# Performance work log

Measured on AMD Instinct MI355X. Metric: run time of the kernel, lower is better.

## Reference

```python
import jax, jax.numpy as jnp
import numpy as np

N = 100000       # num nodes
E = 1600000      # num edges (before self loops)
IN = 128         # in_channels
H = 4            # heads (layer 1)
C = 64           # hidden_channels
BN_EPS = 1e-5
NEG_SLOPE = 0.2  # PyG GATConv default


def setup_inputs() -> dict:
    key = jax.random.key(0)
    ks = jax.random.split(key, 12)
    s = lambda k, shape: jax.random.normal(k, shape, jnp.float32) * 0.05
    return {
        "x": jax.random.normal(ks[0], (N, IN), jnp.float32),
        "edge_index": jax.random.randint(ks[1], (2, E), 0, N),
        # GATConv layer 1: in=128 -> 64 per head, 4 heads, concat
        "W1": s(ks[2], (IN, H * C)),
        "a_src1": s(ks[3], (H, C)),
        "a_dst1": s(ks[4], (H, C)),
        "b1": jnp.zeros((H * C,), jnp.float32),
        # BatchNorm1d(256), eval mode with default running stats
        "bn_gamma": jnp.ones((H * C,), jnp.float32),
        "bn_beta": jnp.zeros((H * C,), jnp.float32),
        # GATConv layer 2: 256 -> 1, heads=1, concat=False
        "W2": s(ks[5], (H * C, 1)),
        "a_src2": s(ks[6], (1, 1)),
        "a_dst2": s(ks[7], (1, 1)),
        "b2": jnp.zeros((1,), jnp.float32),
        # risk predictor MLP: Linear(1,64) -> ReLU -> Linear(64,1) -> Sigmoid
        "mlp_w1": s(ks[8], (1, C)),
        "mlp_b1": jnp.zeros((C,), jnp.float32),
        "mlp_w2": s(ks[9], (C, 1)),
        "mlp_b2": jnp.zeros((1,), jnp.float32),
    }


def gat_conv(x, W, a_s, a_d, b, src, dst, n, concat):
    """PyG-style GATConv (self loops already appended to src/dst)."""
    h_, c_ = a_s.shape
    h = (x @ W).reshape(n, h_, c_)                       # [N,H,C]
    alpha_src = jnp.einsum('nhc,hc->nh', h, a_s)          # [N,H]
    alpha_dst = jnp.einsum('nhc,hc->nh', h, a_d)          # [N,H]
    alpha = jax.nn.leaky_relu(alpha_src[src] + alpha_dst[dst], NEG_SLOPE)  # [E,H]
    # segment softmax over destination nodes (self loops guarantee nonempty segments)
    amax = jax.ops.segment_max(alpha, dst, num_segments=n)
    ex = jnp.exp(alpha - amax[dst])
    den = jax.ops.segment_sum(ex, dst, num_segments=n)
    coef = ex / den[dst]                                  # [E,H]
    out = jax.ops.segment_sum(h[src] * coef[..., None], dst, num_segments=n)  # [N,H,C]
    out = out.reshape(n, h_ * c_) if concat else out.mean(axis=1)
    return out + b


def reference(x, edge_index, W1, a_src1, a_dst1, b1, bn_gamma, bn_beta,
              W2, a_src2, a_dst2, b2, mlp_w1, mlp_b1, mlp_w2, mlp_b2):
    n = x.shape[0]
    loops = jnp.arange(n)
    src = jnp.concatenate([edge_index[0], loops])
    dst = jnp.concatenate([edge_index[1], loops])

    h = gat_conv(x, W1, a_src1, a_dst1, b1, src, dst, n, concat=True)   # [N,256]
    # BatchNorm1d eval: running_mean=0, running_var=1
    h = h / jnp.sqrt(jnp.float32(1.0 + BN_EPS)) * bn_gamma + bn_beta
    h = jax.nn.elu(h)
    # dropout is identity in eval mode
    h = gat_conv(h, W2, a_src2, a_dst2, b2, src, dst, n, concat=False)  # [N,1]

    risk = jax.nn.relu(h @ mlp_w1 + mlp_b1)
    risk = jax.nn.sigmoid(risk @ mlp_w2 + mlp_b2)                        # [N,1]
    return risk
```

## Files before the change

### kernel.cpp

```cpp
#include <hip/hip_runtime.h>
#include <math.h>

#define NSL 0.2f
#define BSH 8
#define CAP 4608
#define ECHUNK 4096
#define MAXNB 512

typedef __attribute__((ext_vector_type(8))) short bf16x8;
typedef __attribute__((ext_vector_type(4))) float f32x4;
typedef __attribute__((ext_vector_type(2))) float floatx2;

__device__ __forceinline__ unsigned short f2b(float f){
  unsigned int u = __builtin_bit_cast(unsigned int, f);
  u = (u + 0x7FFFu + ((u >> 16) & 1u)) >> 16;
  return (unsigned short)u;
}

__global__ void k_binit(int* gCur, int NB){
  int i = blockIdx.x*blockDim.x + threadIdx.x;
  if (i < NB) gCur[i] = i*CAP;
}

__global__ __launch_bounds__(256) void k_bucket(const int* __restrict__ esrc, const int* __restrict__ edst,
                                                int E, int NB, int* gCur, uint2* __restrict__ ebuf){
  __shared__ int hist[MAXNB];
  __shared__ int base[MAXNB];
  int t = threadIdx.x;
  for (int i=t;i<NB;i+=256) hist[i] = 0;
  __syncthreads();
  int e0 = blockIdx.x*ECHUNK;
  int srcv[16], dstv[16];
  #pragma unroll
  for (int j=0;j<16;j++){
    int e = e0 + t + j*256;
    if (e < E){ srcv[j] = esrc[e]; dstv[j] = edst[e]; atomicAdd(&hist[dstv[j]>>BSH], 1); }
    else dstv[j] = -1;
  }
  __syncthreads();
  for (int i=t;i<NB;i+=256){
    int h = hist[i];
    base[i] = h > 0 ? atomicAdd(&gCur[i], h) : 0;
    hist[i] = 0;
  }
  __syncthreads();
  #pragma unroll
  for (int j=0;j<16;j++){
    if (dstv[j] >= 0){
      int b = dstv[j]>>BSH;
      int pos = base[b] + atomicAdd(&hist[b], 1);
      if (pos < (b+1)*CAP)
        ebuf[pos] = (uint2){ (unsigned)srcv[j], (unsigned)dstv[j] };
    }
  }
}

__global__ __launch_bounds__(256) void k_csr(const int* __restrict__ gCur, const uint2* __restrict__ ebuf,
                                             int* __restrict__ rows, int* __restrict__ deg,
                                             int* __restrict__ csr, int N){
  __shared__ int lcnt[256];
  __shared__ int rofs[256];
  __shared__ int csr_l[CAP+256];
  int b = blockIdx.x, t = threadIdx.x;
  int node0 = b<<BSH;
  int nNodes = min(256, N - node0);
  int cnt_b = min(gCur[b] - b*CAP, CAP);
  lcnt[t] = 0;
  __syncthreads();
  const uint2* eb = ebuf + (size_t)b*CAP;
  for (int i=t;i<cnt_b;i+=256) atomicAdd(&lcnt[eb[i].y & 255], 1);
  __syncthreads();
  int v = (t < nNodes) ? (lcnt[t] + 1) : 0;
  rofs[t] = v; __syncthreads();
  #pragma unroll
  for (int o=1;o<256;o<<=1){
    int x = (t>=o) ? rofs[t-o] : 0; __syncthreads();
    rofs[t] += x; __syncthreads();
  }
  int excl = rofs[t] - v;
  if (t < nNodes) csr_l[excl] = node0 + t;
  lcnt[t] = excl + 1;
  __syncthreads();
  for (int i=t;i<cnt_b;i+=256){
    uint2 e = eb[i];
    int pos = atomicAdd(&lcnt[e.y & 255], 1);
    csr_l[pos] = (int)e.x;
  }
  __syncthreads();
  int total = rofs[255];
  int gbase = b*(CAP+256);
  for (int i=t;i<total;i+=256) csr[gbase+i] = csr_l[i];
  if (t < nNodes){ rows[node0+t] = gbase + excl; deg[node0+t] = v; }
}

__global__ void k_prep_x(const float* __restrict__ x, unsigned short* __restrict__ xb, int total8){
  int i = blockIdx.x*blockDim.x + threadIdx.x;
  if (i >= total8) return;
  size_t off = (size_t)i*8;
  float4 a = *(const float4*)&x[off];
  float4 b = *(const float4*)&x[off+4];
  ushort4 lo = { f2b(a.x), f2b(a.y), f2b(a.z), f2b(a.w) };
  ushort4 hi = { f2b(b.x), f2b(b.y), f2b(b.z), f2b(b.w) };
  *(ushort4*)&xb[off]   = lo;
  *(ushort4*)&xb[off+4] = hi;
}

__global__ __launch_bounds__(256) void k_prep_w(const float* __restrict__ W, unsigned short* __restrict__ wt){
  int ch = threadIdx.x;
  for (int k=0;k<128;k++) wt[ch*128 + k] = f2b(W[k*256 + ch]);
}

__global__ __launch_bounds__(256) void k_gemm1(const unsigned short* __restrict__ w1t,
                                               const unsigned short* __restrict__ xb,
                                               const float* __restrict__ a_s1,
                                               const float* __restrict__ a_d1,
                                               unsigned char* __restrict__ h1f8,
                                               float* __restrict__ asrc, float* __restrict__ adst,
                                               int N){
  int tid = threadIdx.x;
  int lane = tid & 63, w = tid >> 6;
  int g = lane >> 4, nr = lane & 15;
  int n0 = blockIdx.x*64;

  f32x4 acc[4][4] = {};
  int node_f[4]; bool val_f[4];
  #pragma unroll
  for (int fn=0;fn<4;fn++){ node_f[fn] = n0 + fn*16 + nr; val_f[fn] = node_f[fn] < N; }

  #pragma unroll
  for (int s=0;s<4;s++){
    int ks = s*32;
    bf16x8 af[4], bf[4];
    #pragma unroll
    for (int fm=0;fm<4;fm++){
      int ch = w*64 + fm*16 + nr;
      const ushort4 lo = *(const ushort4*)(w1t + ch*128 + ks + 4*g);
      const ushort4 hi = *(const ushort4*)(w1t + ch*128 + ks + 16 + 4*g);
      af[fm] = (bf16x8){ (short)lo.x,(short)lo.y,(short)lo.z,(short)lo.w,
                         (short)hi.x,(short)hi.y,(short)hi.z,(short)hi.w };
    }
    #pragma unroll
    for (int fn=0;fn<4;fn++){
      ushort4 lo = {0,0,0,0}, hi = {0,0,0,0};
      if (val_f[fn]){
        const unsigned short* xp = xb + (size_t)node_f[fn]*128 + ks + 4*g;
        lo = *(const ushort4*)xp;
        hi = *(const ushort4*)(xp + 16);
      }
      bf[fn] = (bf16x8){ (short)lo.x,(short)lo.y,(short)lo.z,(short)lo.w,
                         (short)hi.x,(short)hi.y,(short)hi.z,(short)hi.w };
    }
    #pragma unroll
    for (int fm=0;fm<4;fm++)
      #pragma unroll
      for (int fn=0;fn<4;fn++)
        acc[fm][fn] = __builtin_amdgcn_mfma_f32_16x16x32_bf16(af[fm], bf[fn], acc[fm][fn], 0, 0, 0);
  }

  float ps[4] = {0.f,0.f,0.f,0.f}, pd[4] = {0.f,0.f,0.f,0.f};
  #pragma unroll
  for (int fm=0;fm<4;fm++){
    int cb = w*64 + fm*16 + g*4;
    float4 av = *(const float4*)&a_s1[cb];
    float4 dv = *(const float4*)&a_d1[cb];
    #pragma unroll
    for (int fn=0;fn<4;fn++){
      f32x4 c = acc[fm][fn];
      if (val_f[fn]){
        int u = __builtin_amdgcn_cvt_pk_fp8_f32(c[0], c[1], 0, false);
        u = __builtin_amdgcn_cvt_pk_fp8_f32(c[2], c[3], u, true);
        *(unsigned int*)(h1f8 + (size_t)node_f[fn]*256 + cb) = (unsigned int)u;
      }
      ps[fn] += c[0]*av.x + c[1]*av.y + c[2]*av.z + c[3]*av.w;
      pd[fn] += c[0]*dv.x + c[1]*dv.y + c[2]*dv.z + c[3]*dv.w;
    }
  }
  #pragma unroll
  for (int fn=0;fn<4;fn++){
    ps[fn] += __shfl_xor(ps[fn], 16); ps[fn] += __shfl_xor(ps[fn], 32);
    pd[fn] += __shfl_xor(pd[fn], 16); pd[fn] += __shfl_xor(pd[fn], 32);
    if (g == 0 && val_f[fn]){
      asrc[node_f[fn]*4 + w] = ps[fn];
      adst[node_f[fn]*4 + w] = pd[fn];
    }
  }
}

__global__ __launch_bounds__(256) void k_agg1(const int* __restrict__ rows, const int* __restrict__ deg,
                                              const int* __restrict__ csr,
                                              const unsigned char* __restrict__ h1f8,
                                              const float* __restrict__ asrc, const float* __restrict__ adst,
                                              const float* __restrict__ b1,
                                              const float* __restrict__ gamma, const float* __restrict__ beta,
                                              const float* __restrict__ W2,
                                              float* __restrict__ h2, int N){
  int lane = threadIdx.x & 63, wv = threadIdx.x >> 6;
  int node = blockIdx.x*4 + wv;
  if (node >= N) return;
  int slot = lane >> 4, l4 = lane & 15;
  int head = l4 >> 2;
  int rs = rows[node], d = deg[node];
  float adh = adst[node*4 + head];
  const uint4* h1u4 = (const uint4*)h1f8;
  float acc[16];
  #pragma unroll
  for (int j=0;j<16;j++) acc[j] = 0.f;
  float den = 0.f;
  int i = slot;
  if (i < d){
    int s = csr[rs+i];
    float aa = asrc[s*4 + head];
    uint4 v = h1u4[(size_t)s*16 + l4];
    while (true){
      int in = i + 4;
      bool hn = in < d;
      int sn = hn ? csr[rs+in] : 0;
      float al = aa + adh;
      al = (al > 0.f) ? al : NSL*al;
      float wgt = __expf(al);
      den += wgt;
      floatx2 f0 = __builtin_amdgcn_cvt_pk_f32_fp8(v.x, false);
      floatx2 f1 = __builtin_amdgcn_cvt_pk_f32_fp8(v.x, true);
      floatx2 f2 = __builtin_amdgcn_cvt_pk_f32_fp8(v.y, false);
      floatx2 f3 = __builtin_amdgcn_cvt_pk_f32_fp8(v.y, true);
      floatx2 f4 = __builtin_amdgcn_cvt_pk_f32_fp8(v.z, false);
      floatx2 f5 = __builtin_amdgcn_cvt_pk_f32_fp8(v.z, true);
      floatx2 f6 = __builtin_amdgcn_cvt_pk_f32_fp8(v.w, false);
      floatx2 f7 = __builtin_amdgcn_cvt_pk_f32_fp8(v.w, true);
      acc[0] += wgt*f0.x;  acc[1] += wgt*f0.y;  acc[2] += wgt*f1.x;  acc[3] += wgt*f1.y;
      acc[4] += wgt*f2.x;  acc[5] += wgt*f2.y;  acc[6] += wgt*f3.x;  acc[7] += wgt*f3.y;
      acc[8] += wgt*f4.x;  acc[9] += wgt*f4.y;  acc[10]+= wgt*f5.x;  acc[11]+= wgt*f5.y;
      acc[12]+= wgt*f6.x;  acc[13]+= wgt*f6.y;  acc[14]+= wgt*f7.x;  acc[15]+= wgt*f7.y;
      if (!hn) break;
      i = in;
      aa = asrc[sn*4 + head];
      v = h1u4[(size_t)sn*16 + l4];
    }
  }
  #pragma unroll
  for (int j=0;j<16;j++){ acc[j] += __shfl_xor(acc[j],16); acc[j] += __shfl_xor(acc[j],32); }
  den += __shfl_xor(den,16); den += __shfl_xor(den,32);
  float inv = 1.f/den;
  const float bsc = 0.99999500003749968f;
  int c = l4*16;
  float p = 0.f;
  #pragma unroll
  for (int q=0;q<4;q++){
    int cq = c + q*4;
    float4 bb = *(const float4*)&b1[cq];
    float4 gg = *(const float4*)&gamma[cq];
    float4 be = *(const float4*)&beta[cq];
    float4 w2 = *(const float4*)&W2[cq];
    float o0 = (acc[q*4+0]*inv + bb.x)*bsc*gg.x + be.x;
    float o1 = (acc[q*4+1]*inv + bb.y)*bsc*gg.y + be.y;
    float o2 = (acc[q*4+2]*inv + bb.z)*bsc*gg.z + be.z;
    float o3 = (acc[q*4+3]*inv + bb.w)*bsc*gg.w + be.w;
    o0 = (o0>0.f)?o0:(__expf(o0)-1.f); o1 = (o1>0.f)?o1:(__expf(o1)-1.f);
    o2 = (o2>0.f)?o2:(__expf(o2)-1.f); o3 = (o3>0.f)?o3:(__expf(o3)-1.f);
    p += o0*w2.x + o1*w2.y + o2*w2.z + o3*w2.w;
  }
  p += __shfl_xor(p,1); p += __shfl_xor(p,2); p += __shfl_xor(p,4); p += __shfl_xor(p,8);
  if (lane == 0) h2[node] = p;
}

__global__ __launch_bounds__(256) void k_agg2(const int* __restrict__ rows, const int* __restrict__ deg,
                       const int* __restrict__ csr, const float* __restrict__ h2,
                       const float* __restrict__ as2, const float* __restrict__ ad2,
                       const float* __restrict__ b2,
                       const float* __restrict__ mw1, const float* __restrict__ mb1,
                       const float* __restrict__ mw2, const float* __restrict__ mb2,
                       float* __restrict__ out, int N){
  int t = threadIdx.x;
  int g16 = t >> 4, l = t & 15;
  int n = blockIdx.x*16 + g16;
  if (n >= N) return;
  float a_s = as2[0], a_d = ad2[0];
  float hd = h2[n];
  float ad = hd * a_d;
  int rs = rows[n], d = deg[n];
  float den = 0.f, num = 0.f;
  for (int i=l;i<d;i+=16){
    int s = csr[rs+i];
    float hs = h2[s];
    float al = hs*a_s + ad;
    al = (al > 0.f) ? al : NSL*al;
    float w = __expf(al);
    den += w; num += w*hs;
  }
  #pragma unroll
  for (int o=1;o<16;o<<=1){ den += __shfl_xor(den,o); num += __shfl_xor(num,o); }
  float o2 = num/den + b2[0];
  float acc = 0.f;
  #pragma unroll
  for (int q=0;q<4;q++){
    int j = l + q*16;
    float r = fmaxf(o2*mw1[j] + mb1[j], 0.f);
    acc += r*mw2[j];
  }
  #pragma unroll
  for (int o=1;o<16;o<<=1) acc += __shfl_xor(acc,o);
  if (l == 0) out[n] = 1.f/(1.f + __expf(-(acc + mb2[0])));
}

extern "C" void kernel_launch(void* const* d_in, const int* in_sizes, int n_in,
                              void* d_out, int out_size, void* d_ws, size_t ws_size,
                              hipStream_t stream){
  const float* x   = (const float*)d_in[0];
  const int*   ei  = (const int*)  d_in[1];
  const float* W1  = (const float*)d_in[2];
  const float* as1 = (const float*)d_in[3];
  const float* ad1 = (const float*)d_in[4];
  const float* b1  = (const float*)d_in[5];
  const float* gam = (const float*)d_in[6];
  const float* bet = (const float*)d_in[7];
  const float* W2  = (const float*)d_in[8];
  const float* as2 = (const float*)d_in[9];
  const float* ad2 = (const float*)d_in[10];
  const float* b2  = (const float*)d_in[11];
  const float* mw1 = (const float*)d_in[12];
  const float* mb1 = (const float*)d_in[13];
  const float* mw2 = (const float*)d_in[14];
  const float* mb2 = (const float*)d_in[15];
  float* out = (float*)d_out;

  int N = in_sizes[0] / 128;
  int E = in_sizes[1] / 2;
  const int* esrc = ei;
  const int* edst = ei + E;
  int NB = (N + 255) >> 8;

  char* p = (char*)d_ws;
  auto alloc = [&](size_t bytes)->char*{ char* r = p; p += (bytes + 255) & ~(size_t)255; return r; };
  int*   deg   = (int*)  alloc((size_t)N*4);
  int*   rows  = (int*)  alloc((size_t)N*4);
  int*   gCur  = (int*)  alloc((size_t)NB*4);
  uint2* ebuf  = (uint2*)alloc((size_t)NB*CAP*8);
  int*   csr   = (int*)  alloc((size_t)NB*(CAP+256)*4);
  unsigned short* xb   = (unsigned short*)alloc((size_t)N*128*2);
  unsigned short* w1t  = (unsigned short*)alloc((size_t)256*128*2);
  unsigned char*  h1f8 = (unsigned char*) alloc((size_t)N*256);
  float* asrc  = (float*)alloc((size_t)N*4*4);
  float* adst  = (float*)alloc((size_t)N*4*4);
  float* h2    = (float*)alloc((size_t)N*4);

  k_binit<<<(NB+255)/256,256,0,stream>>>(gCur, NB);
  int nbA = (E + ECHUNK - 1)/ECHUNK;
  k_bucket<<<nbA,256,0,stream>>>(esrc, edst, E, NB, gCur, ebuf);
  k_csr   <<<NB,256,0,stream>>>(gCur, ebuf, rows, deg, csr, N);

  int total8 = (N*128)/8;
  k_prep_x<<<(total8+255)/256,256,0,stream>>>(x, xb, total8);
  k_prep_w<<<1,256,0,stream>>>(W1, w1t);

  k_gemm1<<<(N+63)/64,256,0,stream>>>(w1t, xb, as1, ad1, h1f8, asrc, adst, N);

  k_agg1 <<<(N+3)/4,256,0,stream>>>(rows, deg, csr, h1f8, asrc, adst, b1, gam, bet, W2, h2, N);

  k_agg2 <<<(N+15)/16,256,0,stream>>>(rows, deg, csr, h2, as2, ad2, b2, mw1, mb1, mw2, mb2, out, N);
}
```

Before: 256.8 us.

## Fuse x bf16 conversion into GEMM, retile per-wave nodes, packed FMA aggregation

Removes the separate x-to-bf16 pass by loading fp32 x directly in the GEMM and converting with packed bf16 instructions. The GEMM is retiled so each wave owns 16 nodes and all 256 channels, which lets it write all four attention logits per node as one float4. The W1 transpose kernel is parallelised across 128 blocks. The first aggregation loop uses packed FP32 FMA via inline asm, and leaky ReLU becomes a max. W1 fragments are now reloaded by every wave, and the 16 accumulators raise register pressure.

```diff
diff --git a/kernel.cpp b/kernel.cpp
--- a/kernel.cpp
+++ b/kernel.cpp
@@ -15,6 +15,12 @@
   unsigned int u = __builtin_bit_cast(unsigned int, f);
   u = (u + 0x7FFFu + ((u >> 16) & 1u)) >> 16;
   return (unsigned short)u;
+}
+__device__ __forceinline__ unsigned cvtpk_bf16(float a, float b){
+  unsigned r; asm("v_cvt_pk_bf16_f32 %0, %1, %2" : "=v"(r) : "v"(a), "v"(b)); return r;
+}
+__device__ __forceinline__ void pkfma(floatx2& a, floatx2 x, floatx2 w){
+  asm("v_pk_fma_f32 %0, %1, %2, %0" : "+v"(a) : "v"(x), "v"(w));
 }
 
 __global__ void k_binit(int* gCur, int NB){
@@ -93,96 +99,73 @@
   if (t < nNodes){ rows[node0+t] = gbase + excl; deg[node0+t] = v; }
 }
 
-__global__ void k_prep_x(const float* __restrict__ x, unsigned short* __restrict__ xb, int total8){
-  int i = blockIdx.x*blockDim.x + threadIdx.x;
-  if (i >= total8) return;
-  size_t off = (size_t)i*8;
-  float4 a = *(const float4*)&x[off];
-  float4 b = *(const float4*)&x[off+4];
-  ushort4 lo = { f2b(a.x), f2b(a.y), f2b(a.z), f2b(a.w) };
-  ushort4 hi = { f2b(b.x), f2b(b.y), f2b(b.z), f2b(b.w) };
-  *(ushort4*)&xb[off]   = lo;
-  *(ushort4*)&xb[off+4] = hi;
-}
-
 __global__ __launch_bounds__(256) void k_prep_w(const float* __restrict__ W, unsigned short* __restrict__ wt){
-  int ch = threadIdx.x;
-  for (int k=0;k<128;k++) wt[ch*128 + k] = f2b(W[k*256 + ch]);
+  int idx = blockIdx.x*256 + threadIdx.x;
+  int k = idx >> 8, ch = idx & 255;
+  wt[ch*128 + k] = f2b(W[idx]);
 }
 
 __global__ __launch_bounds__(256) void k_gemm1(const unsigned short* __restrict__ w1t,
-                                               const unsigned short* __restrict__ xb,
+                                               const float* __restrict__ x,
                                                const float* __restrict__ a_s1,
                                                const float* __restrict__ a_d1,
                                                unsigned char* __restrict__ h1f8,
-                                               float* __restrict__ asrc, float* __restrict__ adst,
+                                               float* __restrict__ as4, float* __restrict__ ad4,
                                                int N){
   int tid = threadIdx.x;
   int lane = tid & 63, w = tid >> 6;
   int g = lane >> 4, nr = lane & 15;
-  int n0 = blockIdx.x*64;
-
-  f32x4 acc[4][4] = {};
-  int node_f[4]; bool val_f[4];
-  #pragma unroll
-  for (int fn=0;fn<4;fn++){ node_f[fn] = n0 + fn*16 + nr; val_f[fn] = node_f[fn] < N; }
-
-  #pragma unroll
-  for (int s=0;s<4;s++){
-    int ks = s*32;
-    bf16x8 af[4], bf[4];
+  int node = blockIdx.x*64 + w*16 + nr;
+  bool val = node < N;
+
+  f32x4 acc[16] = {};
+  #pragma unroll
+  for (int ks=0;ks<4;ks++){
+    float4 xlo = make_float4(0,0,0,0), xhi = xlo;
+    if (val){
+      const float* xp = x + (size_t)node*128 + ks*32 + 4*g;
+      xlo = *(const float4*)xp;
+      xhi = *(const float4*)(xp + 16);
+    }
+    union { unsigned u[4]; bf16x8 v; } bb;
+    bb.u[0] = cvtpk_bf16(xlo.x, xlo.y);
+    bb.u[1] = cvtpk_bf16(xlo.z, xlo.w);
+    bb.u[2] = cvtpk_bf16(xhi.x, xhi.y);
+    bb.u[3] = cvtpk_bf16(xhi.z, xhi.w);
     #pragma unroll
-    for (int fm=0;fm<4;fm++){
-      int ch = w*64 + fm*16 + nr;
-      const ushort4 lo = *(const ushort4*)(w1t + ch*128 + ks + 4*g);
-      const ushort4 hi = *(const ushort4*)(w1t + ch*128 + ks + 16 + 4*g);
-      af[fm] = (bf16x8){ (short)lo.x,(short)lo.y,(short)lo.z,(short)lo.w,
-                         (short)hi.x,(short)hi.y,(short)hi.z,(short)hi.w };
-    }
-    #pragma unroll
-    for (int fn=0;fn<4;fn++){
-      ushort4 lo = {0,0,0,0}, hi = {0,0,0,0};
-      if (val_f[fn]){
-        const unsigned short* xp = xb + (size_t)node_f[fn]*128 + ks + 4*g;
-        lo = *(const ushort4*)xp;
-        hi = *(const ushort4*)(xp + 16);
-      }
-      bf[fn] = (bf16x8){ (short)lo.x,(short)lo.y,(short)lo.z,(short)lo.w,
-                         (short)hi.x,(short)hi.y,(short)hi.z,(short)hi.w };
-    }
-    #pragma unroll
-    for (int fm=0;fm<4;fm++)
-      #pragma unroll
-      for (int fn=0;fn<4;fn++)
-        acc[fm][fn] = __builtin_amdgcn_mfma_f32_16x16x32_bf16(af[fm], bf[fn], acc[fm][fn], 0, 0, 0);
-  }
-
-  float ps[4] = {0.f,0.f,0.f,0.f}, pd[4] = {0.f,0.f,0.f,0.f};
-  #pragma unroll
-  for (int fm=0;fm<4;fm++){
-    int cb = w*64 + fm*16 + g*4;
+    for (int fm=0;fm<16;fm++){
+      int ch = fm*16 + nr;
+      const ushort4 lo = *(const ushort4*)(w1t + ch*128 + ks*32 + 4*g);
+      const ushort4 hi = *(const ushort4*)(w1t + ch*128 + ks*32 + 16 + 4*g);
+      bf16x8 a = { (short)lo.x,(short)lo.y,(short)lo.z,(short)lo.w,
+                   (short)hi.x,(short)hi.y,(short)hi.z,(short)hi.w };
+      acc[fm] = __builtin_amdgcn_mfma_f32_16x16x32_bf16(a, bb.v, acc[fm], 0, 0, 0);
+    }
+  }
+
+  float ps[4] = {0,0,0,0}, pd[4] = {0,0,0,0};
+  #pragma unroll
+  for (int fm=0;fm<16;fm++){
+    int cb = fm*16 + g*4;
     float4 av = *(const float4*)&a_s1[cb];
     float4 dv = *(const float4*)&a_d1[cb];
-    #pragma unroll
-    for (int fn=0;fn<4;fn++){
-      f32x4 c = acc[fm][fn];
-      if (val_f[fn]){
-        int u = __builtin_amdgcn_cvt_pk_fp8_f32(c[0], c[1], 0, false);
-        u = __builtin_amdgcn_cvt_pk_fp8_f32(c[2], c[3], u, true);
-        *(unsigned int*)(h1f8 + (size_t)node_f[fn]*256 + cb) = (unsigned int)u;
-      }
-      ps[fn] += c[0]*av.x + c[1]*av.y + c[2]*av.z + c[3]*av.w;
-      pd[fn] += c[0]*dv.x + c[1]*dv.y + c[2]*dv.z + c[3]*dv.w;
-    }
-  }
-  #pragma unroll
-  for (int fn=0;fn<4;fn++){
-    ps[fn] += __shfl_xor(ps[fn], 16); ps[fn] += __shfl_xor(ps[fn], 32);
-    pd[fn] += __shfl_xor(pd[fn], 16); pd[fn] += __shfl_xor(pd[fn], 32);
-    if (g == 0 && val_f[fn]){
-      asrc[node_f[fn]*4 + w] = ps[fn];
-      adst[node_f[fn]*4 + w] = pd[fn];
-    }
+    f32x4 c = acc[fm];
+    if (val){
+      int u = __builtin_amdgcn_cvt_pk_fp8_f32(c[0], c[1], 0, false);
+      u = __builtin_amdgcn_cvt_pk_fp8_f32(c[2], c[3], u, true);
+      *(unsigned int*)(h1f8 + (size_t)node*256 + cb) = (unsigned int)u;
+    }
+    ps[fm>>2] += c[0]*av.x + c[1]*av.y + c[2]*av.z + c[3]*av.w;
+    pd[fm>>2] += c[0]*dv.x + c[1]*dv.y + c[2]*dv.z + c[3]*dv.w;
+  }
+  #pragma unroll
+  for (int h=0;h<4;h++){
+    ps[h] += __shfl_xor(ps[h], 16); ps[h] += __shfl_xor(ps[h], 32);
+    pd[h] += __shfl_xor(pd[h], 16); pd[h] += __shfl_xor(pd[h], 32);
+  }
+  if (g == 0 && val){
+    *(float4*)&as4[(size_t)node*4] = make_float4(ps[0], ps[1], ps[2], ps[3]);
+    *(float4*)&ad4[(size_t)node*4] = make_float4(pd[0], pd[1], pd[2], pd[3]);
   }
 }
 
@@ -202,9 +185,9 @@
   int rs = rows[node], d = deg[node];
   float adh = adst[node*4 + head];
   const uint4* h1u4 = (const uint4*)h1f8;
-  float acc[16];
-  #pragma unroll
-  for (int j=0;j<16;j++) acc[j] = 0.f;
+  floatx2 acc2[8];
+  #pragma unroll
+  for (int j=0;j<8;j++){ acc2[j][0] = 0.f; acc2[j][1] = 0.f; }
   float den = 0.f;
   int i = slot;
   if (i < d){
@@ -216,21 +199,19 @@
       bool hn = in < d;
       int sn = hn ? csr[rs+in] : 0;
       float al = aa + adh;
-      al = (al > 0.f) ? al : NSL*al;
+      al = fmaxf(al, NSL*al);
       float wgt = __expf(al);
       den += wgt;
-      floatx2 f0 = __builtin_amdgcn_cvt_pk_f32_fp8(v.x, false);
-      floatx2 f1 = __builtin_amdgcn_cvt_pk_f32_fp8(v.x, true);
-      floatx2 f2 = __builtin_amdgcn_cvt_pk_f32_fp8(v.y, false);
-      floatx2 f3 = __builtin_amdgcn_cvt_pk_f32_fp8(v.y, true);
-      floatx2 f4 = __builtin_amdgcn_cvt_pk_f32_fp8(v.z, false);
-      floatx2 f5 = __builtin_amdgcn_cvt_pk_f32_fp8(v.z, true);
-      floatx2 f6 = __builtin_amdgcn_cvt_pk_f32_fp8(v.w, false);
-      floatx2 f7 = __builtin_amdgcn_cvt_pk_f32_fp8(v.w, true);
-      acc[0] += wgt*f0.x;  acc[1] += wgt*f0.y;  acc[2] += wgt*f1.x;  acc[3] += wgt*f1.y;
-      acc[4] += wgt*f2.x;  acc[5] += wgt*f2.y;  acc[6] += wgt*f3.x;  acc[7] += wgt*f3.y;
-      acc[8] += wgt*f4.x;  acc[9] += wgt*f4.y;  acc[10]+= wgt*f5.x;  acc[11]+= wgt*f5.y;
-      acc[12]+= wgt*f6.x;  acc[13]+= wgt*f6.y;  acc[14]+= wgt*f7.x;  acc[15]+= wgt*f7.y;
+      floatx2 ww; ww[0] = wgt; ww[1] = wgt;
+      floatx2 f;
+      f = __builtin_amdgcn_cvt_pk_f32_fp8(v.x, false); pkfma(acc2[0], f, ww);
+      f = __builtin_amdgcn_cvt_pk_f32_fp8(v.x, true ); pkfma(acc2[1], f, ww);
+      f = __builtin_amdgcn_cvt_pk_f32_fp8(v.y, false); pkfma(acc2[2], f, ww);
+      f = __builtin_amdgcn_cvt_pk_f32_fp8(v.y, true ); pkfma(acc2[3], f, ww);
+      f = __builtin_amdgcn_cvt_pk_f32_fp8(v.z, false); pkfma(acc2[4], f, ww);
+      f = __builtin_amdgcn_cvt_pk_f32_fp8(v.z, true ); pkfma(acc2[5], f, ww);
+      f = __builtin_amdgcn_cvt_pk_f32_fp8(v.w, false); pkfma(acc2[6], f, ww);
+      f = __builtin_amdgcn_cvt_pk_f32_fp8(v.w, true ); pkfma(acc2[7], f, ww);
       if (!hn) break;
       i = in;
       aa = asrc[sn*4 + head];
@@ -238,7 +219,10 @@
     }
   }
   #pragma unroll
-  for (int j=0;j<16;j++){ acc[j] += __shfl_xor(acc[j],16); acc[j] += __shfl_xor(acc[j],32); }
+  for (int j=0;j<8;j++){
+    acc2[j][0] += __shfl_xor(acc2[j][0],16); acc2[j][1] += __shfl_xor(acc2[j][1],16);
+    acc2[j][0] += __shfl_xor(acc2[j][0],32); acc2[j][1] += __shfl_xor(acc2[j][1],32);
+  }
   den += __shfl_xor(den,16); den += __shfl_xor(den,32);
   float inv = 1.f/den;
   const float bsc = 0.99999500003749968f;
@@ -251,10 +235,10 @@
     float4 gg = *(const float4*)&gamma[cq];
     float4 be = *(const float4*)&beta[cq];
     float4 w2 = *(const float4*)&W2[cq];
-    float o0 = (acc[q*4+0]*inv + bb.x)*bsc*gg.x + be.x;
-    float o1 = (acc[q*4+1]*inv + bb.y)*bsc*gg.y + be.y;
-    float o2 = (acc[q*4+2]*inv + bb.z)*bsc*gg.z + be.z;
-    float o3 = (acc[q*4+3]*inv + bb.w)*bsc*gg.w + be.w;
+    float o0 = (acc2[q*2+0][0]*inv + bb.x)*bsc*gg.x + be.x;
+    float o1 = (acc2[q*2+0][1]*inv + bb.y)*bsc*gg.y + be.y;
+    float o2 = (acc2[q*2+1][0]*inv + bb.z)*bsc*gg.z + be.z;
+    float o3 = (acc2[q*2+1][1]*inv + bb.w)*bsc*gg.w + be.w;
     o0 = (o0>0.f)?o0:(__expf(o0)-1.f); o1 = (o1>0.f)?o1:(__expf(o1)-1.f);
     o2 = (o2>0.f)?o2:(__expf(o2)-1.f); o3 = (o3>0.f)?o3:(__expf(o3)-1.f);
     p += o0*w2.x + o1*w2.y + o2*w2.z + o3*w2.w;
@@ -283,7 +267,7 @@
     int s = csr[rs+i];
     float hs = h2[s];
     float al = hs*a_s + ad;
-    al = (al > 0.f) ? al : NSL*al;
+    al = fmaxf(al, NSL*al);
     float w = __expf(al);
     den += w; num += w*hs;
   }
@@ -336,7 +320,6 @@
   int*   gCur  = (int*)  alloc((size_t)NB*4);
   uint2* ebuf  = (uint2*)alloc((size_t)NB*CAP*8);
   int*   csr   = (int*)  alloc((size_t)NB*(CAP+256)*4);
-  unsigned short* xb   = (unsigned short*)alloc((size_t)N*128*2);
   unsigned short* w1t  = (unsigned short*)alloc((size_t)256*128*2);
   unsigned char*  h1f8 = (unsigned char*) alloc((size_t)N*256);
   float* asrc  = (float*)alloc((size_t)N*4*4);
@@ -348,11 +331,9 @@
   k_bucket<<<nbA,256,0,stream>>>(esrc, edst, E, NB, gCur, ebuf);
   k_csr   <<<NB,256,0,stream>>>(gCur, ebuf, rows, deg, csr, N);
 
-  int total8 = (N*128)/8;
-  k_prep_x<<<(total8+255)/256,256,0,stream>>>(x, xb, total8);
-  k_prep_w<<<1,256,0,stream>>>(W1, w1t);
-
-  k_gemm1<<<(N+63)/64,256,0,stream>>>(w1t, xb, as1, ad1, h1f8, asrc, adst, N);
+  k_prep_w<<<128,256,0,stream>>>(W1, w1t);
+
+  k_gemm1<<<(N+63)/64,256,0,stream>>>(w1t, x, as1, ad1, h1f8, asrc, adst, N);
 
   k_agg1 <<<(N+3)/4,256,0,stream>>>(rows, deg, csr, h1f8, asrc, adst, b1, gam, bet, W2, h2, N);
 
```

Result: slower. 307.2 us (+19.6%).
